# Performance work log

Hardware: AMD Instinct MI355X
Metric: run time of the kernel (lower is better)

Reference implementation:

```python
import jax, jax.numpy as jnp
import numpy as np

# Scalar-only irreps: 8x0e nodes in, 4x0e edge in, 8x0e edge out, 16x0e node out.
N = 50000          # nodes
E = 800000         # edges
MUL_NODE_IN = 8
MUL_EDGE_IN = 4
MUL_Z = 2 * MUL_NODE_IN          # cat([x[i], x[j]]) -> 16
MUL_EDGE_OUT = 8
MUL_NODE_OUT = 16
W_NUMEL = MUL_EDGE_IN * MUL_Z * MUL_EDGE_OUT  # 512 = edge_tp.weight_numel
RAD_IN, RAD_HID = 16, 64         # radial_neurons=[16, 64]


def setup_inputs() -> dict:
    key = jax.random.key(0)
    ks = jax.random.split(key, 7)
    x = jax.random.normal(ks[0], (N, MUL_NODE_IN), dtype=jnp.float32)
    edge_index = jax.random.randint(ks[1], (2, E), 0, N)
    edge_attr = jax.random.normal(ks[2], (E, MUL_EDGE_IN), dtype=jnp.float32)
    edge_len_emb = jax.random.normal(ks[3], (E, RAD_IN), dtype=jnp.float32)
    # radial MLP (e3nn FullyConnectedNet: normalized linear layers, silu)
    w1 = jax.random.normal(ks[4], (RAD_IN, RAD_HID), dtype=jnp.float32)
    w2 = jax.random.normal(ks[5], (RAD_HID, W_NUMEL), dtype=jnp.float32)
    # node_tp internal shared weights: [mul_node_in, mul_edge_out, mul_node_out]
    w_node = jax.random.normal(ks[6], (MUL_NODE_IN, MUL_EDGE_OUT, MUL_NODE_OUT), dtype=jnp.float32)
    return {"x": x, "edge_index": edge_index, "edge_attr": edge_attr,
            "edge_len_emb": edge_len_emb, "w1": w1, "w2": w2, "w_node": w_node}


def reference(x, edge_index, edge_attr, edge_len_emb, w1, w2, w_node):
    i, j = edge_index[0], edge_index[1]
    # radial MLP -> per-edge TP weights (e3nn normalized linears, silu)
    h = jax.nn.silu(edge_len_emb @ w1 / jnp.sqrt(jnp.float32(RAD_IN)))
    w_edge = (h @ w2 / jnp.sqrt(jnp.float32(RAD_HID)))
    w_edge = w_edge.reshape(E, MUL_EDGE_IN, MUL_Z, MUL_EDGE_OUT)
    # gather + concat: z = cat([x[i], x[j]])  [E, 16]
    z = jnp.concatenate([x[i], x[j]], axis=-1)
    # edge_tp: fully-connected scalar TP with path norm 1/sqrt(mul1*mul2)
    edge_out = jnp.einsum('ea,eb,eabk->ek', edge_attr, z, w_edge)
    edge_out = edge_out / jnp.sqrt(jnp.float32(MUL_EDGE_IN * MUL_Z))
    # scatter-sum to destination nodes j
    e_sum = jax.ops.segment_sum(edge_out, j, num_segments=x.shape[0])
    # node_tp: shared internal weights, path norm 1/sqrt(mul1*mul2)
    x_out = jnp.einsum('na,nb,abk->nk', x, e_sum, w_node)
    x_out = x_out / jnp.sqrt(jnp.float32(MUL_NODE_IN * MUL_EDGE_OUT))
    return (x_out, edge_out)
```

## Files before the change

kernel.cpp:

```cpp
#include <hip/hip_runtime.h>


typedef __attribute__((ext_vector_type(8))) short short8;
typedef __attribute__((ext_vector_type(4))) float floatx4;

__device__ inline unsigned short f2bf(float f) {
    union { float f; unsigned u; } v; v.f = f;
    unsigned r = v.u + 0x7FFFu + ((v.u >> 16) & 1u);
    return (unsigned short)(r >> 16);
}
__device__ inline float bf2f(unsigned short u) {
    union { unsigned u; float f; } v; v.u = ((unsigned)u) << 16;
    return v.f;
}

__device__ inline unsigned cvt_pk_bf16(float lo, float hi) {
    unsigned r;
    asm("v_cvt_pk_bf16_f32 %0, %1, %2" : "=v"(r) : "v"(lo), "v"(hi));
    return r;
}

constexpr int TB    = 512;
constexpr int NBLK  = 512;
constexpr int NWAVE = TB / 64;

constexpr int AT_LDF = 32;

__global__ __launch_bounds__(TB, 2)
void edge_kernel(
    const float* __restrict__ x,
    const int*   __restrict__ ei,
    const float* __restrict__ attr,
    const float* __restrict__ emb,
    const float* __restrict__ w1,
    const float* __restrict__ w2,
    float* __restrict__ edge_out,
    float* __restrict__ e_sum,
    int E)
{
    __shared__ __align__(16) unsigned short s_w2t[512 * 64];
    __shared__ __align__(16) unsigned short s_ztA[NWAVE * 16 * 32];
    __shared__ __align__(16) float          s_atA[NWAVE * 4 * AT_LDF];
    __shared__ int                          s_vjA[NWAVE * 32];

    const int tid  = threadIdx.x;
    const int wave = tid >> 6;
    const int lane = tid & 63;
    const int m16  = lane & 15;
    const int quad = lane >> 4;
    const int par  = m16 >> 3;

    for (int idx = tid; idx < 512 * 64; idx += TB) {
        const int n = idx & 511, k = idx >> 9;
        s_w2t[n * 64 + (k ^ ((n & 7) << 3))] = f2bf(w2[k * 512 + n]);
    }
    __syncthreads();

    short8 w1f[4];
    #pragma unroll
    for (int mt = 0; mt < 4; ++mt) {
        short8 f;
        if (quad < 2) {
            #pragma unroll
            for (int j = 0; j < 8; ++j)
                f[j] = (short)f2bf(w1[(quad * 8 + j) * 64 + mt * 16 + m16]);
        } else {
            #pragma unroll
            for (int j = 0; j < 8; ++j) f[j] = 0;
        }
        w1f[mt] = f;
    }

    unsigned short* ztw = s_ztA + wave * 16 * 32;
    float*          atw = s_atA + wave * 4 * AT_LDF;
    int*            vjw = s_vjA + wave * 32;

    const int  wid = blockIdx.x * NWAVE + wave;
    const int  nw  = NBLK * NWAVE;
    const int  ntiles = E >> 5;
    const bool stg = (quad < 2);
    const int  mst = quad * 16 + m16;

    const int srcA = m16 + 16 * ((2 * quad) & 3);
    const int srcB = m16 + 16 * ((2 * quad + 1) & 3);

    const int swz = (m16 & 7) << 3;
    const int o0  = (quad * 8) ^ swz;
    const int o1  = o0 ^ 32;

    float4 xi0, xi1, xj0, xj1, a4;
    float4 em0a, em0b, em1a, em1b;
    int viN = 0, vjN = 0, vjC = 0;

    if (wid < ntiles && stg) {
        const int e0 = (wid << 5) + mst;
        const int vi = ei[e0];
        vjC = ei[E + e0];
        xi0 = *(const float4*)(x + (size_t)vi * 8);
        xi1 = *(const float4*)(x + (size_t)vi * 8 + 4);
        xj0 = *(const float4*)(x + (size_t)vjC * 8);
        xj1 = *(const float4*)(x + (size_t)vjC * 8 + 4);
        a4  = *(const float4*)(attr + (size_t)e0 * 4);
        const float* ep0 = emb + (size_t)((wid << 5) + m16) * 16 + quad * 8;
        em0a = *(const float4*)ep0;
        em0b = *(const float4*)(ep0 + 4);
        const float* ep1 = emb + (size_t)((wid << 5) + 16 + m16) * 16 + quad * 8;
        em1a = *(const float4*)ep1;
        em1b = *(const float4*)(ep1 + 4);
        const int t1 = (wid + nw < ntiles) ? (wid + nw) : wid;
        const int e1 = (t1 << 5) + mst;
        viN = ei[e1];
        vjN = ei[E + e1];
    }

    for (int tile = wid; tile < ntiles; tile += nw) {
        const int base = tile << 5;

        if (stg) {
            unsigned w;
            w = cvt_pk_bf16(xi0.x, xi0.y);
            ztw[ 0*32+mst] = (unsigned short)w; ztw[ 1*32+mst] = (unsigned short)(w >> 16);
            w = cvt_pk_bf16(xi0.z, xi0.w);
            ztw[ 2*32+mst] = (unsigned short)w; ztw[ 3*32+mst] = (unsigned short)(w >> 16);
            w = cvt_pk_bf16(xi1.x, xi1.y);
            ztw[ 4*32+mst] = (unsigned short)w; ztw[ 5*32+mst] = (unsigned short)(w >> 16);
            w = cvt_pk_bf16(xi1.z, xi1.w);
            ztw[ 6*32+mst] = (unsigned short)w; ztw[ 7*32+mst] = (unsigned short)(w >> 16);
            w = cvt_pk_bf16(xj0.x, xj0.y);
            ztw[ 8*32+mst] = (unsigned short)w; ztw[ 9*32+mst] = (unsigned short)(w >> 16);
            w = cvt_pk_bf16(xj0.z, xj0.w);
            ztw[10*32+mst] = (unsigned short)w; ztw[11*32+mst] = (unsigned short)(w >> 16);
            w = cvt_pk_bf16(xj1.x, xj1.y);
            ztw[12*32+mst] = (unsigned short)w; ztw[13*32+mst] = (unsigned short)(w >> 16);
            w = cvt_pk_bf16(xj1.z, xj1.w);
            ztw[14*32+mst] = (unsigned short)w; ztw[15*32+mst] = (unsigned short)(w >> 16);
            atw[0*AT_LDF+mst]=a4.x;   atw[1*AT_LDF+mst]=a4.y;
            atw[2*AT_LDF+mst]=a4.z;   atw[3*AT_LDF+mst]=a4.w;
            vjw[mst] = vjC;
        }

        short8 a1[2];
        {
            union { short8 s8; unsigned u[4]; } uu;
            if (stg) {
                uu.u[0] = cvt_pk_bf16(em0a.x, em0a.y);
                uu.u[1] = cvt_pk_bf16(em0a.z, em0a.w);
                uu.u[2] = cvt_pk_bf16(em0b.x, em0b.y);
                uu.u[3] = cvt_pk_bf16(em0b.z, em0b.w);
            } else {
                uu.u[0]=0u; uu.u[1]=0u; uu.u[2]=0u; uu.u[3]=0u;
            }
            a1[0] = uu.s8;
            if (stg) {
                uu.u[0] = cvt_pk_bf16(em1a.x, em1a.y);
                uu.u[1] = cvt_pk_bf16(em1a.z, em1a.w);
                uu.u[2] = cvt_pk_bf16(em1b.x, em1b.y);
                uu.u[3] = cvt_pk_bf16(em1b.z, em1b.w);
            } else {
                uu.u[0]=0u; uu.u[1]=0u; uu.u[2]=0u; uu.u[3]=0u;
            }
            a1[1] = uu.s8;
        }

        {
            const int tn     = tile + nw;
            const int tn_cl  = (tn  < ntiles) ? tn  : tile;
            const int tnn    = tn + nw;
            const int tnn_cl = (tnn < ntiles) ? tnn : tn_cl;
            if (stg) {
                const int en = (tn_cl << 5) + mst;
                vjC = vjN;
                xi0 = *(const float4*)(x + (size_t)viN * 8);
                xi1 = *(const float4*)(x + (size_t)viN * 8 + 4);
                xj0 = *(const float4*)(x + (size_t)vjN * 8);
                xj1 = *(const float4*)(x + (size_t)vjN * 8 + 4);
                a4  = *(const float4*)(attr + (size_t)en * 4);
                const float* ep0 = emb + (size_t)((tn_cl << 5) + m16) * 16 + quad * 8;
                em0a = *(const float4*)ep0;
                em0b = *(const float4*)(ep0 + 4);
                const float* ep1 = emb + (size_t)((tn_cl << 5) + 16 + m16) * 16 + quad * 8;
                em1a = *(const float4*)ep1;
                em1b = *(const float4*)(ep1 + 4);
                const int enn = (tnn_cl << 5) + mst;
                viN = ei[enn];
                vjN = ei[E + enn];
            }
        }

        short8 a2[2][2];
        #pragma unroll
        for (int s = 0; s < 2; ++s) {
            unsigned p[4][2];
            #pragma unroll
            for (int half = 0; half < 2; ++half) {
                floatx4 c0, c1;
                {
                    floatx4 z4 = {0.f, 0.f, 0.f, 0.f};
                    c0 = __builtin_amdgcn_mfma_f32_16x16x32_bf16(w1f[2*half    ], a1[s], z4, 0, 0, 0);
                    c1 = __builtin_amdgcn_mfma_f32_16x16x32_bf16(w1f[2*half + 1], a1[s], z4, 0, 0, 0);
                }
                #pragma unroll
                for (int h = 0; h < 2; ++h) {
                    const floatx4& c = h ? c1 : c0;
                    float sv[4];
                    #pragma unroll
                    for (int r = 0; r < 4; ++r) {
                        const float u   = c[r] * 0.25f;
                        const float den = 1.f + __expf(-u);
                        sv[r] = u * __builtin_amdgcn_rcpf(den) * 0.015625f;
                    }
                    p[2*half + h][0] = cvt_pk_bf16(sv[0], sv[1]);
                    p[2*half + h][1] = cvt_pk_bf16(sv[2], sv[3]);
                }
            }
            #pragma unroll
            for (int qq = 0; qq < 2; ++qq) {
                union { short8 s8; unsigned u[4]; } uu;
                #pragma unroll
                for (int w = 0; w < 4; ++w) {
                    const int srcLane = (w < 2) ? srcA : srcB;
                    const unsigned vA = (unsigned)__shfl((int)p[2*qq    ][w & 1], srcLane, 64);
                    const unsigned vB = (unsigned)__shfl((int)p[2*qq + 1][w & 1], srcLane, 64);
                    uu.u[w] = (quad & 2) ? vB : vA;
                }
                a2[s][qq] = uu.s8;
            }
        }

        float eacc[2][4];
        #pragma unroll
        for (int s = 0; s < 2; ++s)
            #pragma unroll
            for (int r = 0; r < 4; ++r) eacc[s][r] = 0.f;

        __builtin_amdgcn_s_setprio(1);
        #pragma unroll 1
        for (int g = 0; g < 4; ++g) {
            float av[2][4];
            #pragma unroll
            for (int s = 0; s < 2; ++s) {
                const float4 a4v = *(const float4*)(atw + g * AT_LDF + s * 16 + quad * 4);
                av[s][0] = a4v.x; av[s][1] = a4v.y;
                av[s][2] = a4v.z; av[s][3] = a4v.w;
            }

            float tacc[2][4];
            #pragma unroll
            for (int s = 0; s < 2; ++s)
                #pragma unroll
                for (int r = 0; r < 4; ++r) tacc[s][r] = 0.f;

            #pragma unroll
            for (int tt = 0; tt < 8; ++tt) {
                const int t = g * 8 + tt;
                const unsigned short* wrow = s_w2t + (16 * t + m16) * 64;
                short8 b2[2];
                b2[0] = *(const short8*)(wrow + o0);
                b2[1] = *(const short8*)(wrow + o1);
                const int b_idx = (2 * tt + par) & 15;
                #pragma unroll
                for (int s = 0; s < 2; ++s) {
                    floatx4 c = {0.f, 0.f, 0.f, 0.f};
                    c = __builtin_amdgcn_mfma_f32_16x16x32_bf16(a2[s][0], b2[0], c, 0, 0, 0);
                    c = __builtin_amdgcn_mfma_f32_16x16x32_bf16(a2[s][1], b2[1], c, 0, 0, 0);
                    const ushort4 zu = *(const ushort4*)(ztw + b_idx * 32 + s * 16 + quad * 4);
                    tacc[s][0] = fmaf(c[0], bf2f(zu.x), tacc[s][0]);
                    tacc[s][1] = fmaf(c[1], bf2f(zu.y), tacc[s][1]);
                    tacc[s][2] = fmaf(c[2], bf2f(zu.z), tacc[s][2]);
                    tacc[s][3] = fmaf(c[3], bf2f(zu.w), tacc[s][3]);
                }
            }
            #pragma unroll
            for (int s = 0; s < 2; ++s)
                #pragma unroll
                for (int r = 0; r < 4; ++r)
                    eacc[s][r] = fmaf(av[s][r], tacc[s][r], eacc[s][r]);
        }
        __builtin_amdgcn_s_setprio(0);

        #pragma unroll
        for (int s = 0; s < 2; ++s)
            #pragma unroll
            for (int r = 0; r < 4; ++r)
                eacc[s][r] += __shfl_xor(eacc[s][r], 8, 64);

        if (m16 < 8) {
            #pragma unroll
            for (int s = 0; s < 2; ++s) {
                const int4 vjq = *(const int4*)(vjw + s * 16 + quad * 4);
                const int vjr[4] = {vjq.x, vjq.y, vjq.z, vjq.w};
                #pragma unroll
                for (int r = 0; r < 4; ++r) {
                    const int e = base + s * 16 + quad * 4 + r;
                    edge_out[(size_t)e * 8 + m16] = eacc[s][r];
                    atomicAdd(e_sum + (size_t)vjr[r] * 8 + m16, eacc[s][r]);
                }
            }
        }
    }
}

__global__ __launch_bounds__(256) void node_kernel(
    const float* __restrict__ x,
    const float* __restrict__ e_sum,
    const float* __restrict__ w_node,
    float* __restrict__ x_out,
    int N)
{
    __shared__ float s_w[8 * 8 * 16];
    for (int idx = threadIdx.x; idx < 1024; idx += 256) s_w[idx] = w_node[idx];
    __syncthreads();

    const int n = blockIdx.x * 256 + threadIdx.x;
    if (n >= N) return;

    float xa[8], eb[8];
    #pragma unroll
    for (int a = 0; a < 8; ++a) xa[a] = x[(size_t)n * 8 + a];
    #pragma unroll
    for (int b = 0; b < 8; ++b) eb[b] = e_sum[(size_t)n * 8 + b];

    float out[16];
    #pragma unroll
    for (int k = 0; k < 16; ++k) out[k] = 0.f;

    const float4* wv = (const float4*)s_w;
    #pragma unroll
    for (int a = 0; a < 8; ++a) {
        #pragma unroll
        for (int b = 0; b < 8; ++b) {
            const float t = xa[a] * eb[b] * 0.125f;
            #pragma unroll
            for (int k4 = 0; k4 < 4; ++k4) {
                const float4 w = wv[(a * 8 + b) * 4 + k4];
                out[k4 * 4 + 0] = fmaf(t, w.x, out[k4 * 4 + 0]);
                out[k4 * 4 + 1] = fmaf(t, w.y, out[k4 * 4 + 1]);
                out[k4 * 4 + 2] = fmaf(t, w.z, out[k4 * 4 + 2]);
                out[k4 * 4 + 3] = fmaf(t, w.w, out[k4 * 4 + 3]);
            }
        }
    }

    float4* xo = (float4*)(x_out + (size_t)n * 16);
    #pragma unroll
    for (int k4 = 0; k4 < 4; ++k4)
        xo[k4] = make_float4(out[k4 * 4 + 0], out[k4 * 4 + 1],
                             out[k4 * 4 + 2], out[k4 * 4 + 3]);
}

extern "C" void kernel_launch(void* const* d_in, const int* in_sizes, int n_in,
                              void* d_out, int out_size, void* d_ws, size_t ws_size,
                              hipStream_t stream) {
    const float* x      = (const float*)d_in[0];
    const int*   ei     = (const int*)d_in[1];
    const float* attr   = (const float*)d_in[2];
    const float* emb    = (const float*)d_in[3];
    const float* w1     = (const float*)d_in[4];
    const float* w2     = (const float*)d_in[5];
    const float* w_node = (const float*)d_in[6];

    const int N = in_sizes[0] / 8;
    const int E = in_sizes[2] / 4;

    float* x_out    = (float*)d_out;
    float* edge_out = (float*)d_out + (size_t)N * 16;
    float* e_sum    = (float*)d_ws;

    hipMemsetAsync(e_sum, 0, (size_t)N * 8 * sizeof(float), stream);

    edge_kernel<<<NBLK, TB, 0, stream>>>(x, ei, attr, emb, w1, w2,
                                         edge_out, e_sum, E);

    node_kernel<<<(N + 255) / 256, 256, 0, stream>>>(x, e_sum, w_node, x_out, N);
}
```

Before: 198.0 us.

## Software-pipeline radial MLP of next tile with current tile's edge TP

New measurement: 408.0 us. 106% more time.

```diff
diff --git a/kernel.cpp b/kernel.cpp
--- a/kernel.cpp
+++ b/kernel.cpp
@@ -4,27 +4,163 @@
 typedef __attribute__((ext_vector_type(8))) short short8;
 typedef __attribute__((ext_vector_type(4))) float floatx4;
 
-__device__ inline unsigned short f2bf(float f) {
+#define AI __attribute__((always_inline))
+
+__device__ AI inline unsigned short f2bf(float f) {
     union { float f; unsigned u; } v; v.f = f;
     unsigned r = v.u + 0x7FFFu + ((v.u >> 16) & 1u);
     return (unsigned short)(r >> 16);
 }
-__device__ inline float bf2f(unsigned short u) {
+__device__ AI inline float bf2f(unsigned short u) {
     union { unsigned u; float f; } v; v.u = ((unsigned)u) << 16;
     return v.f;
 }
-
-__device__ inline unsigned cvt_pk_bf16(float lo, float hi) {
+__device__ AI inline unsigned cvt_pk_bf16(float lo, float hi) {
     unsigned r;
     asm("v_cvt_pk_bf16_f32 %0, %1, %2" : "=v"(r) : "v"(lo), "v"(hi));
     return r;
 }
 
 constexpr int TB    = 512;
-constexpr int NBLK  = 512;
+constexpr int NBLK  = 256;
 constexpr int NWAVE = TB / 64;
 
-constexpr int AT_LDF = 32;
+__device__ AI inline void c_build(const short8 (&w1f)[4], const short8& a1s,
+                                  const int srcA, const int srcB, const bool selB,
+                                  short8& q0, short8& q1)
+{
+    unsigned p[4][2];
+    #pragma unroll
+    for (int half = 0; half < 2; ++half) {
+        floatx4 z4 = {0.f, 0.f, 0.f, 0.f};
+        floatx4 c0 = __builtin_amdgcn_mfma_f32_16x16x32_bf16(w1f[2*half    ], a1s, z4, 0, 0, 0);
+        floatx4 c1 = __builtin_amdgcn_mfma_f32_16x16x32_bf16(w1f[2*half + 1], a1s, z4, 0, 0, 0);
+        #pragma unroll
+        for (int h = 0; h < 2; ++h) {
+            const floatx4& c = h ? c1 : c0;
+            float sv[4];
+            #pragma unroll
+            for (int r = 0; r < 4; ++r) {
+                const float u   = c[r] * 0.25f;
+                const float den = 1.f + __expf(-u);
+                sv[r] = u * __builtin_amdgcn_rcpf(den) * 0.015625f;
+            }
+            p[2*half + h][0] = cvt_pk_bf16(sv[0], sv[1]);
+            p[2*half + h][1] = cvt_pk_bf16(sv[2], sv[3]);
+        }
+    }
+    #pragma unroll
+    for (int qq = 0; qq < 2; ++qq) {
+        union { short8 s8; unsigned u[4]; } uu;
+        #pragma unroll
+        for (int w = 0; w < 4; ++w) {
+            const int srcLane = (w < 2) ? srcA : srcB;
+            const unsigned vA = (unsigned)__shfl((int)p[2*qq    ][w & 1], srcLane, 64);
+            const unsigned vB = (unsigned)__shfl((int)p[2*qq + 1][w & 1], srcLane, 64);
+            uu.u[w] = selB ? vB : vA;
+        }
+        if (qq == 0) q0 = uu.s8; else q1 = uu.s8;
+    }
+}
+
+__device__ AI inline void d_group(const unsigned short* __restrict__ w2t,
+                                  const unsigned short* __restrict__ zt,
+                                  const float* __restrict__ at,
+                                  const int g, const int m16, const int quad, const int par,
+                                  const int o0, const int o1,
+                                  const short8& a00, const short8& a01,
+                                  const short8& a10, const short8& a11,
+                                  float (&eacc)[2][4])
+{
+    float av[2][4];
+    #pragma unroll
+    for (int s = 0; s < 2; ++s) {
+        const float4 a4v = *(const float4*)(at + g * 32 + s * 16 + quad * 4);
+        av[s][0] = a4v.x; av[s][1] = a4v.y; av[s][2] = a4v.z; av[s][3] = a4v.w;
+    }
+    float tacc[2][4];
+    #pragma unroll
+    for (int s = 0; s < 2; ++s)
+        #pragma unroll
+        for (int r = 0; r < 4; ++r) tacc[s][r] = 0.f;
+
+    #pragma unroll
+    for (int tt = 0; tt < 8; ++tt) {
+        const int t = g * 8 + tt;
+        const unsigned short* wrow = w2t + (16 * t + m16) * 64;
+        const short8 b20 = *(const short8*)(wrow + o0);
+        const short8 b21 = *(const short8*)(wrow + o1);
+        const int b_idx = (2 * tt + par) & 15;
+        {
+            floatx4 c = {0.f, 0.f, 0.f, 0.f};
+            c = __builtin_amdgcn_mfma_f32_16x16x32_bf16(a00, b20, c, 0, 0, 0);
+            c = __builtin_amdgcn_mfma_f32_16x16x32_bf16(a01, b21, c, 0, 0, 0);
+            const ushort4 zu = *(const ushort4*)(zt + b_idx * 32 + quad * 4);
+            tacc[0][0] = fmaf(c[0], bf2f(zu.x), tacc[0][0]);
+            tacc[0][1] = fmaf(c[1], bf2f(zu.y), tacc[0][1]);
+            tacc[0][2] = fmaf(c[2], bf2f(zu.z), tacc[0][2]);
+            tacc[0][3] = fmaf(c[3], bf2f(zu.w), tacc[0][3]);
+        }
+        {
+            floatx4 c = {0.f, 0.f, 0.f, 0.f};
+            c = __builtin_amdgcn_mfma_f32_16x16x32_bf16(a10, b20, c, 0, 0, 0);
+            c = __builtin_amdgcn_mfma_f32_16x16x32_bf16(a11, b21, c, 0, 0, 0);
+            const ushort4 zu = *(const ushort4*)(zt + b_idx * 32 + 16 + quad * 4);
+            tacc[1][0] = fmaf(c[0], bf2f(zu.x), tacc[1][0]);
+            tacc[1][1] = fmaf(c[1], bf2f(zu.y), tacc[1][1]);
+            tacc[1][2] = fmaf(c[2], bf2f(zu.z), tacc[1][2]);
+            tacc[1][3] = fmaf(c[3], bf2f(zu.w), tacc[1][3]);
+        }
+    }
+    #pragma unroll
+    for (int s = 0; s < 2; ++s)
+        #pragma unroll
+        for (int r = 0; r < 4; ++r)
+            eacc[s][r] = fmaf(av[s][r], tacc[s][r], eacc[s][r]);
+}
+
+__device__ AI inline void stage_write(unsigned short* __restrict__ zt,
+                                      float* __restrict__ at, int* __restrict__ vjw,
+                                      const int mst,
+                                      const float4& xi0, const float4& xi1,
+                                      const float4& xj0, const float4& xj1,
+                                      const float4& a4, const int vj)
+{
+    unsigned w;
+    w = cvt_pk_bf16(xi0.x, xi0.y);
+    zt[ 0*32+mst] = (unsigned short)w; zt[ 1*32+mst] = (unsigned short)(w >> 16);
+    w = cvt_pk_bf16(xi0.z, xi0.w);
+    zt[ 2*32+mst] = (unsigned short)w; zt[ 3*32+mst] = (unsigned short)(w >> 16);
+    w = cvt_pk_bf16(xi1.x, xi1.y);
+    zt[ 4*32+mst] = (unsigned short)w; zt[ 5*32+mst] = (unsigned short)(w >> 16);
+    w = cvt_pk_bf16(xi1.z, xi1.w);
+    zt[ 6*32+mst] = (unsigned short)w; zt[ 7*32+mst] = (unsigned short)(w >> 16);
+    w = cvt_pk_bf16(xj0.x, xj0.y);
+    zt[ 8*32+mst] = (unsigned short)w; zt[ 9*32+mst] = (unsigned short)(w >> 16);
+    w = cvt_pk_bf16(xj0.z, xj0.w);
+    zt[10*32+mst] = (unsigned short)w; zt[11*32+mst] = (unsigned short)(w >> 16);
+    w = cvt_pk_bf16(xj1.x, xj1.y);
+    zt[12*32+mst] = (unsigned short)w; zt[13*32+mst] = (unsigned short)(w >> 16);
+    w = cvt_pk_bf16(xj1.z, xj1.w);
+    zt[14*32+mst] = (unsigned short)w; zt[15*32+mst] = (unsigned short)(w >> 16);
+    at[0*32+mst] = a4.x; at[1*32+mst] = a4.y;
+    at[2*32+mst] = a4.z; at[3*32+mst] = a4.w;
+    vjw[mst] = vj;
+}
+
+__device__ AI inline short8 pack_a1(const float4& u0, const float4& u1, const bool stg)
+{
+    union { short8 s8; unsigned u[4]; } uu;
+    if (stg) {
+        uu.u[0] = cvt_pk_bf16(u0.x, u0.y);
+        uu.u[1] = cvt_pk_bf16(u0.z, u0.w);
+        uu.u[2] = cvt_pk_bf16(u1.x, u1.y);
+        uu.u[3] = cvt_pk_bf16(u1.z, u1.w);
+    } else {
+        uu.u[0] = 0u; uu.u[1] = 0u; uu.u[2] = 0u; uu.u[3] = 0u;
+    }
+    return uu.s8;
+}
 
 __global__ __launch_bounds__(TB, 2)
 void edge_kernel(
@@ -39,9 +175,9 @@
     int E)
 {
     __shared__ __align__(16) unsigned short s_w2t[512 * 64];
-    __shared__ __align__(16) unsigned short s_ztA[NWAVE * 16 * 32];
-    __shared__ __align__(16) float          s_atA[NWAVE * 4 * AT_LDF];
-    __shared__ int                          s_vjA[NWAVE * 32];
+    __shared__ __align__(16) unsigned short s_ztA[NWAVE * 2 * 512];
+    __shared__ __align__(16) float          s_atA[NWAVE * 2 * 128];
+    __shared__ int                          s_vjA[NWAVE * 2 * 32];
 
     const int tid  = threadIdx.x;
     const int wave = tid >> 6;
@@ -71,160 +207,84 @@
         w1f[mt] = f;
     }
 
-    unsigned short* ztw = s_ztA + wave * 16 * 32;
-    float*          atw = s_atA + wave * 4 * AT_LDF;
-    int*            vjw = s_vjA + wave * 32;
+    unsigned short* ztw0 = s_ztA + (wave * 2    ) * 512;
+    unsigned short* ztw1 = s_ztA + (wave * 2 + 1) * 512;
+    float*          atw0 = s_atA + (wave * 2    ) * 128;
+    float*          atw1 = s_atA + (wave * 2 + 1) * 128;
+    int*            vjw0 = s_vjA + (wave * 2    ) * 32;
+    int*            vjw1 = s_vjA + (wave * 2 + 1) * 32;
 
     const int  wid = blockIdx.x * NWAVE + wave;
     const int  nw  = NBLK * NWAVE;
     const int  ntiles = E >> 5;
     const bool stg = (quad < 2);
     const int  mst = quad * 16 + m16;
+    const bool selB = (quad & 2);
 
     const int srcA = m16 + 16 * ((2 * quad) & 3);
     const int srcB = m16 + 16 * ((2 * quad + 1) & 3);
-
     const int swz = (m16 & 7) << 3;
     const int o0  = (quad * 8) ^ swz;
     const int o1  = o0 ^ 32;
 
-    float4 xi0, xi1, xj0, xj1, a4;
-    float4 em0a, em0b, em1a, em1b;
-    int viN = 0, vjN = 0, vjC = 0;
-
-    if (wid < ntiles && stg) {
-        const int e0 = (wid << 5) + mst;
-        const int vi = ei[e0];
-        vjC = ei[E + e0];
-        xi0 = *(const float4*)(x + (size_t)vi * 8);
-        xi1 = *(const float4*)(x + (size_t)vi * 8 + 4);
-        xj0 = *(const float4*)(x + (size_t)vjC * 8);
-        xj1 = *(const float4*)(x + (size_t)vjC * 8 + 4);
-        a4  = *(const float4*)(attr + (size_t)e0 * 4);
-        const float* ep0 = emb + (size_t)((wid << 5) + m16) * 16 + quad * 8;
-        em0a = *(const float4*)ep0;
-        em0b = *(const float4*)(ep0 + 4);
-        const float* ep1 = emb + (size_t)((wid << 5) + 16 + m16) * 16 + quad * 8;
-        em1a = *(const float4*)ep1;
-        em1b = *(const float4*)(ep1 + 4);
-        const int t1 = (wid + nw < ntiles) ? (wid + nw) : wid;
-        const int e1 = (t1 << 5) + mst;
-        viN = ei[e1];
-        vjN = ei[E + e1];
-    }
-
+    int viC = 0, vjC = 0;
+    short8 a2c[2][2];
+    {
+        float4 xi0, xi1, xj0, xj1, a4;
+        float4 em0a, em0b, em1a, em1b;
+        if (stg) {
+            const int e0 = (wid << 5) + mst;
+            const int vi = ei[e0];
+            const int vj = ei[E + e0];
+            xi0 = *(const float4*)(x + (size_t)vi * 8);
+            xi1 = *(const float4*)(x + (size_t)vi * 8 + 4);
+            xj0 = *(const float4*)(x + (size_t)vj * 8);
+            xj1 = *(const float4*)(x + (size_t)vj * 8 + 4);
+            a4  = *(const float4*)(attr + (size_t)e0 * 4);
+            const float* ep0 = emb + (size_t)((wid << 5) + m16) * 16 + quad * 8;
+            em0a = *(const float4*)ep0;
+            em0b = *(const float4*)(ep0 + 4);
+            const float* ep1 = emb + (size_t)((wid << 5) + 16 + m16) * 16 + quad * 8;
+            em1a = *(const float4*)ep1;
+            em1b = *(const float4*)(ep1 + 4);
+            stage_write(ztw0, atw0, vjw0, mst, xi0, xi1, xj0, xj1, a4, vj);
+            const int t1 = (wid + nw < ntiles) ? (wid + nw) : wid;
+            const int e1 = (t1 << 5) + mst;
+            viC = ei[e1];
+            vjC = ei[E + e1];
+        }
+        const short8 a1s0 = pack_a1(em0a, em0b, stg);
+        const short8 a1s1 = pack_a1(em1a, em1b, stg);
+        c_build(w1f, a1s0, srcA, srcB, selB, a2c[0][0], a2c[0][1]);
+        c_build(w1f, a1s1, srcA, srcB, selB, a2c[1][0], a2c[1][1]);
+    }
+
+    int cur = 0;
     for (int tile = wid; tile < ntiles; tile += nw) {
-        const int base = tile << 5;
-
+        const int base  = tile << 5;
+        const int tn_cl = (tile + nw < ntiles) ? (tile + nw) : tile;
+        unsigned short* zt_c = cur ? ztw1 : ztw0;
+        unsigned short* zt_n = cur ? ztw0 : ztw1;
+        float*          at_c = cur ? atw1 : atw0;
+        float*          at_n = cur ? atw0 : atw1;
+        int*            vj_c = cur ? vjw1 : vjw0;
+        int*            vj_n = cur ? vjw0 : vjw1;
+
+        float4 xi0, xi1, xj0, xj1, a4;
+        float4 em0a, em0b, em1a, em1b;
         if (stg) {
-            unsigned w;
-            w = cvt_pk_bf16(xi0.x, xi0.y);
-            ztw[ 0*32+mst] = (unsigned short)w; ztw[ 1*32+mst] = (unsigned short)(w >> 16);
-            w = cvt_pk_bf16(xi0.z, xi0.w);
-            ztw[ 2*32+mst] = (unsigned short)w; ztw[ 3*32+mst] = (unsigned short)(w >> 16);
-            w = cvt_pk_bf16(xi1.x, xi1.y);
-            ztw[ 4*32+mst] = (unsigned short)w; ztw[ 5*32+mst] = (unsigned short)(w >> 16);
-            w = cvt_pk_bf16(xi1.z, xi1.w);
-            ztw[ 6*32+mst] = (unsigned short)w; ztw[ 7*32+mst] = (unsigned short)(w >> 16);
-            w = cvt_pk_bf16(xj0.x, xj0.y);
-            ztw[ 8*32+mst] = (unsigned short)w; ztw[ 9*32+mst] = (unsigned short)(w >> 16);
-            w = cvt_pk_bf16(xj0.z, xj0.w);
-            ztw[10*32+mst] = (unsigned short)w; ztw[11*32+mst] = (unsigned short)(w >> 16);
-            w = cvt_pk_bf16(xj1.x, xj1.y);
-            ztw[12*32+mst] = (unsigned short)w; ztw[13*32+mst] = (unsigned short)(w >> 16);
-            w = cvt_pk_bf16(xj1.z, xj1.w);
-            ztw[14*32+mst] = (unsigned short)w; ztw[15*32+mst] = (unsigned short)(w >> 16);
-            atw[0*AT_LDF+mst]=a4.x;   atw[1*AT_LDF+mst]=a4.y;
-            atw[2*AT_LDF+mst]=a4.z;   atw[3*AT_LDF+mst]=a4.w;
-            vjw[mst] = vjC;
-        }
-
-        short8 a1[2];
-        {
-            union { short8 s8; unsigned u[4]; } uu;
-            if (stg) {
-                uu.u[0] = cvt_pk_bf16(em0a.x, em0a.y);
-                uu.u[1] = cvt_pk_bf16(em0a.z, em0a.w);
-                uu.u[2] = cvt_pk_bf16(em0b.x, em0b.y);
-                uu.u[3] = cvt_pk_bf16(em0b.z, em0b.w);
-            } else {
-                uu.u[0]=0u; uu.u[1]=0u; uu.u[2]=0u; uu.u[3]=0u;
-            }
-            a1[0] = uu.s8;
-            if (stg) {
-                uu.u[0] = cvt_pk_bf16(em1a.x, em1a.y);
-                uu.u[1] = cvt_pk_bf16(em1a.z, em1a.w);
-                uu.u[2] = cvt_pk_bf16(em1b.x, em1b.y);
-                uu.u[3] = cvt_pk_bf16(em1b.z, em1b.w);
-            } else {
-                uu.u[0]=0u; uu.u[1]=0u; uu.u[2]=0u; uu.u[3]=0u;
-            }
-            a1[1] = uu.s8;
-        }
-
-        {
-            const int tn     = tile + nw;
-            const int tn_cl  = (tn  < ntiles) ? tn  : tile;
-            const int tnn    = tn + nw;
-            const int tnn_cl = (tnn < ntiles) ? tnn : tn_cl;
-            if (stg) {
-                const int en = (tn_cl << 5) + mst;
-                vjC = vjN;
-                xi0 = *(const float4*)(x + (size_t)viN * 8);
-                xi1 = *(const float4*)(x + (size_t)viN * 8 + 4);
-                xj0 = *(const float4*)(x + (size_t)vjN * 8);
-                xj1 = *(const float4*)(x + (size_t)vjN * 8 + 4);
-                a4  = *(const float4*)(attr + (size_t)en * 4);
-                const float* ep0 = emb + (size_t)((tn_cl << 5) + m16) * 16 + quad * 8;
-                em0a = *(const float4*)ep0;
-                em0b = *(const float4*)(ep0 + 4);
-                const float* ep1 = emb + (size_t)((tn_cl << 5) + 16 + m16) * 16 + quad * 8;
-                em1a = *(const float4*)ep1;
-                em1b = *(const float4*)(ep1 + 4);
-                const int enn = (tnn_cl << 5) + mst;
-                viN = ei[enn];
-                vjN = ei[E + enn];
-            }
-        }
-
-        short8 a2[2][2];
-        #pragma unroll
-        for (int s = 0; s < 2; ++s) {
-            unsigned p[4][2];
-            #pragma unroll
-            for (int half = 0; half < 2; ++half) {
-                floatx4 c0, c1;
-                {
-                    floatx4 z4 = {0.f, 0.f, 0.f, 0.f};
-                    c0 = __builtin_amdgcn_mfma_f32_16x16x32_bf16(w1f[2*half    ], a1[s], z4, 0, 0, 0);
-                    c1 = __builtin_amdgcn_mfma_f32_16x16x32_bf16(w1f[2*half + 1], a1[s], z4, 0, 0, 0);
-                }
-                #pragma unroll
-                for (int h = 0; h < 2; ++h) {
-                    const floatx4& c = h ? c1 : c0;
-                    float sv[4];
-                    #pragma unroll
-                    for (int r = 0; r < 4; ++r) {
-                        const float u   = c[r] * 0.25f;
-                        const float den = 1.f + __expf(-u);
-                        sv[r] = u * __builtin_amdgcn_rcpf(den) * 0.015625f;
-                    }
-                    p[2*half + h][0] = cvt_pk_bf16(sv[0], sv[1]);
-                    p[2*half + h][1] = cvt_pk_bf16(sv[2], sv[3]);
-                }
-            }
-            #pragma unroll
-            for (int qq = 0; qq < 2; ++qq) {
-                union { short8 s8; unsigned u[4]; } uu;
-                #pragma unroll
-                for (int w = 0; w < 4; ++w) {
-                    const int srcLane = (w < 2) ? srcA : srcB;
-                    const unsigned vA = (unsigned)__shfl((int)p[2*qq    ][w & 1], srcLane, 64);
-                    const unsigned vB = (unsigned)__shfl((int)p[2*qq + 1][w & 1], srcLane, 64);
-                    uu.u[w] = (quad & 2) ? vB : vA;
-                }
-                a2[s][qq] = uu.s8;
-            }
+            const int en = (tn_cl << 5) + mst;
+            xi0 = *(const float4*)(x + (size_t)viC * 8);
+            xi1 = *(const float4*)(x + (size_t)viC * 8 + 4);
+            xj0 = *(const float4*)(x + (size_t)vjC * 8);
+            xj1 = *(const float4*)(x + (size_t)vjC * 8 + 4);
+            a4  = *(const float4*)(attr + (size_t)en * 4);
+            const float* ep0 = emb + (size_t)((tn_cl << 5) + m16) * 16 + quad * 8;
+            em0a = *(const float4*)ep0;
+            em0b = *(const float4*)(ep0 + 4);
+            const float* ep1 = emb + (size_t)((tn_cl << 5) + 16 + m16) * 16 + quad * 8;
+            em1a = *(const float4*)ep1;
+            em1b = *(const float4*)(ep1 + 4);
         }
 
         float eacc[2][4];
@@ -233,50 +293,28 @@
             #pragma unroll
             for (int r = 0; r < 4; ++r) eacc[s][r] = 0.f;
 
-        __builtin_amdgcn_s_setprio(1);
-        #pragma unroll 1
-        for (int g = 0; g < 4; ++g) {
-            float av[2][4];
-            #pragma unroll
-            for (int s = 0; s < 2; ++s) {
-                const float4 a4v = *(const float4*)(atw + g * AT_LDF + s * 16 + quad * 4);
-                av[s][0] = a4v.x; av[s][1] = a4v.y;
-                av[s][2] = a4v.z; av[s][3] = a4v.w;
-            }
-
-            float tacc[2][4];
-            #pragma unroll
-            for (int s = 0; s < 2; ++s)
-                #pragma unroll
-                for (int r = 0; r < 4; ++r) tacc[s][r] = 0.f;
-
-            #pragma unroll
-            for (int tt = 0; tt < 8; ++tt) {
-                const int t = g * 8 + tt;
-                const unsigned short* wrow = s_w2t + (16 * t + m16) * 64;
-                short8 b2[2];
-                b2[0] = *(const short8*)(wrow + o0);
-                b2[1] = *(const short8*)(wrow + o1);
-                const int b_idx = (2 * tt + par) & 15;
-                #pragma unroll
-                for (int s = 0; s < 2; ++s) {
-                    floatx4 c = {0.f, 0.f, 0.f, 0.f};
-                    c = __builtin_amdgcn_mfma_f32_16x16x32_bf16(a2[s][0], b2[0], c, 0, 0, 0);
-                    c = __builtin_amdgcn_mfma_f32_16x16x32_bf16(a2[s][1], b2[1], c, 0, 0, 0);
-                    const ushort4 zu = *(const ushort4*)(ztw + b_idx * 32 + s * 16 + quad * 4);
-                    tacc[s][0] = fmaf(c[0], bf2f(zu.x), tacc[s][0]);
-                    tacc[s][1] = fmaf(c[1], bf2f(zu.y), tacc[s][1]);
-                    tacc[s][2] = fmaf(c[2], bf2f(zu.z), tacc[s][2]);
-                    tacc[s][3] = fmaf(c[3], bf2f(zu.w), tacc[s][3]);
-                }
-            }
-            #pragma unroll
-            for (int s = 0; s < 2; ++s)
-                #pragma unroll
-                for (int r = 0; r < 4; ++r)
-                    eacc[s][r] = fmaf(av[s][r], tacc[s][r], eacc[s][r]);
-        }
-        __builtin_amdgcn_s_setprio(0);
+        d_group(s_w2t, zt_c, at_c, 0, m16, quad, par, o0, o1,
+                a2c[0][0], a2c[0][1], a2c[1][0], a2c[1][1], eacc);
+        d_group(s_w2t, zt_c, at_c, 1, m16, quad, par, o0, o1,
+                a2c[0][0], a2c[0][1], a2c[1][0], a2c[1][1], eacc);
+
+        if (stg) {
+            stage_write(zt_n, at_n, vj_n, mst, xi0, xi1, xj0, xj1, a4, vjC);
+            const int t2 = (tile + 2 * nw < ntiles) ? (tile + 2 * nw) : tn_cl;
+            const int e2 = (t2 << 5) + mst;
+            viC = ei[e2];
+            vjC = ei[E + e2];
+        }
+        const short8 a1s0 = pack_a1(em0a, em0b, stg);
+        const short8 a1s1 = pack_a1(em1a, em1b, stg);
+
+        short8 a2n[2][2];
+        c_build(w1f, a1s0, srcA, srcB, selB, a2n[0][0], a2n[0][1]);
+        d_group(s_w2t, zt_c, at_c, 2, m16, quad, par, o0, o1,
+                a2c[0][0], a2c[0][1], a2c[1][0], a2c[1][1], eacc);
+        c_build(w1f, a1s1, srcA, srcB, selB, a2n[1][0], a2n[1][1]);
+        d_group(s_w2t, zt_c, at_c, 3, m16, quad, par, o0, o1,
+                a2c[0][0], a2c[0][1], a2c[1][0], a2c[1][1], eacc);
 
         #pragma unroll
         for (int s = 0; s < 2; ++s)
@@ -287,7 +325,7 @@
         if (m16 < 8) {
             #pragma unroll
             for (int s = 0; s < 2; ++s) {
-                const int4 vjq = *(const int4*)(vjw + s * 16 + quad * 4);
+                const int4 vjq = *(const int4*)(vj_c + s * 16 + quad * 4);
                 const int vjr[4] = {vjq.x, vjq.y, vjq.z, vjq.w};
                 #pragma unroll
                 for (int r = 0; r < 4; ++r) {
@@ -297,6 +335,10 @@
                 }
             }
         }
+
+        a2c[0][0] = a2n[0][0]; a2c[0][1] = a2n[0][1];
+        a2c[1][0] = a2n[1][0]; a2c[1][1] = a2n[1][1];
+        cur ^= 1;
     }
 }
 
```
